# Optimization experiments

Measured on AMD Instinct MI355X. Metric: run time of the kernel, lower is better.

## Reference

```python
import jax, jax.numpy as jnp
import numpy as np

N_USERS = 50000
N0, N1, N2 = 200000, 50000, 12500
E0, E1, E2 = 1600000, 400000, 100000
B = 128
NUMP, TWEET, CATP, DES = 6, 768, 2, 768
IN_DIM, HID = 128, 128
SLOPE = 0.01  # LeakyReLU default


def setup_inputs() -> dict:
    key = jax.random.key(0)
    ks = iter(jax.random.split(key, 32))
    f32 = jnp.float32
    nrm = lambda s, sc=0.05: jax.random.normal(next(ks), s, f32) * sc
    inp = {}
    inp['x_raw'] = jax.random.normal(next(ks), (N_USERS, NUMP + TWEET + CATP + DES), f32)
    inp['W_des'] = nrm((DES, IN_DIM // 4)); inp['b_des'] = jnp.zeros((IN_DIM // 4,), f32)
    inp['W_tweet'] = nrm((TWEET, IN_DIM // 4)); inp['b_tweet'] = jnp.zeros((IN_DIM // 4,), f32)
    inp['W_num'] = nrm((NUMP, IN_DIM // 4)); inp['b_num'] = jnp.zeros((IN_DIM // 4,), f32)
    inp['W_cat'] = nrm((CATP, IN_DIM // 4)); inp['b_cat'] = jnp.zeros((IN_DIM // 4,), f32)
    inp['W_in'] = nrm((IN_DIM, HID)); inp['b_in'] = jnp.zeros((HID,), f32)
    inp['prelu_a'] = jnp.full((HID,), 0.25, f32)
    inp['W_conv'] = nrm((3, HID, HID)); inp['b_conv'] = jnp.zeros((3, HID), f32)
    inp['Wc1'] = nrm((3 * HID, HID)); inp['bc1'] = jnp.zeros((HID,), f32)
    inp['Wc2'] = nrm((HID, HID)); inp['bc2'] = jnp.zeros((HID,), f32)
    ri = lambda n, hi: jax.random.randint(next(ks), (n,), 0, hi, jnp.int32)
    inp['nodelist'] = ri(N0, N_USERS)
    inp['e0'] = jnp.stack([ri(E0, N0), ri(E0, N0)])
    inp['e1'] = jnp.stack([ri(E1, N1), ri(E1, N1)])
    inp['e2'] = jnp.stack([ri(E2, N2), ri(E2, N2)])
    inp['parent1'] = ri(N0, N1)   # coarsening assignment layer0 -> layer1
    inp['parent2'] = ri(N1, N2)   # layer1 -> layer2
    inp['batch1'] = jnp.sort(ri(N1, B))
    inp['batch2'] = jnp.sort(ri(N2, B))
    return inp


def _leaky(x):
    return jnp.where(x > 0, x, SLOPE * x)


def _gcn(h, ei, W, b, n):
    # GCNConv: lin -> sym-normalized add-aggregation with self-loops -> +bias
    h = h @ W
    loop = jnp.arange(n, dtype=ei.dtype)
    src = jnp.concatenate([ei[0], loop])
    dst = jnp.concatenate([ei[1], loop])
    deg = jax.ops.segment_sum(jnp.ones(dst.shape, h.dtype), dst, num_segments=n)
    dinv = jnp.where(deg > 0, jax.lax.rsqrt(deg), 0.0)
    msg = h[src] * (dinv[src] * dinv[dst])[:, None]
    return jax.ops.segment_sum(msg, dst, num_segments=n) + b


def reference(x_raw, W_des, b_des, W_tweet, b_tweet, W_num, b_num, W_cat, b_cat,
              W_in, b_in, prelu_a, W_conv, b_conv, Wc1, bc1, Wc2, bc2,
              nodelist, e0, e1, e2, parent1, parent2, batch1, batch2):
    # FeatureEncoder (twibot-20 slicing order: num_prop | tweet | cat_prop | des)
    n = _leaky(x_raw[:, :NUMP] @ W_num + b_num)
    t = _leaky(x_raw[:, NUMP:NUMP + TWEET] @ W_tweet + b_tweet)
    c = _leaky(x_raw[:, NUMP + TWEET:NUMP + TWEET + CATP] @ W_cat + b_cat)
    d = _leaky(x_raw[:, NUMP + TWEET + CATP:] @ W_des + b_des)
    h = jnp.concatenate([d, t, n, c], axis=1) @ W_in + b_in
    enc = jnp.where(h > 0, h, prelu_a * h)  # PReLU

    x = enc[nodelist]  # [N0, HID] gather per batched nodelists
    edges = [e0, e1, e2]
    sizes = [N0, N1, N2]
    parents = [parent1, parent2]
    nxt = [N1, N2]
    xs = []
    for i in range(3):
        x = jax.nn.relu(_gcn(x, edges[i], W_conv[i], b_conv[i], sizes[i]))
        if i < 2:  # SEPooling: pure scatter-add onto parent nodes (nn unused in its forward)
            x = jax.nn.relu(jax.ops.segment_sum(x, parents[i], num_segments=nxt[i]))
        xs.append(x)
    pooled = jnp.concatenate([
        jax.ops.segment_sum(xs[0], batch1, num_segments=B),
        jax.ops.segment_sum(xs[1], batch2, num_segments=B),
        jax.ops.segment_sum(xs[2], batch2, num_segments=B),
    ], axis=1)  # global sum pool, batch at layer min(i+1, tree_depth-1)
    z = jax.nn.relu(pooled @ Wc1 + bc1)  # dropout inactive (eval)
    return z @ Wc2 + bc2
```

## Files before the change

kernel.cpp:

```cpp
#include <hip/hip_runtime.h>

#define N_USERS 50000
#define NN0 200000
#define NN1 50000
#define NN2 12500
#define EE0 1600000
#define EE1 400000
#define EE2 100000


__global__ __launch_bounds__(256) void k_enc3(
    const float* __restrict__ xr,
    const float* __restrict__ Wd, const float* __restrict__ bd,
    const float* __restrict__ Wt, const float* __restrict__ bt,
    const float* __restrict__ Wn, const float* __restrict__ bn,
    const float* __restrict__ Wc, const float* __restrict__ bc,
    float* __restrict__ h128)
{
    __shared__ float XsB[4368];
    __shared__ float Ws[32][68];
    __shared__ float xnc[64][8];
    __shared__ float Wl[8][64];

    int t = threadIdx.x;
    int lane = t & 63, wv = t >> 6;
    int cg = t & 15, rg = t >> 4;
    int base = blockIdx.x * 64;

    if (t < 64) {
        int row = base + t;
        if (row < N_USERS) {
            const float* xp = xr + (size_t)row * 1544;
            float4 a = *(const float4*)xp;
            float2 b2 = *(const float2*)(xp + 4);
            float2 c2 = *(const float2*)(xp + 774);
            xnc[t][0] = a.x; xnc[t][1] = a.y; xnc[t][2] = a.z; xnc[t][3] = a.w;
            xnc[t][4] = b2.x; xnc[t][5] = b2.y; xnc[t][6] = c2.x; xnc[t][7] = c2.y;
        } else {
            #pragma unroll
            for (int k = 0; k < 8; k++) xnc[t][k] = 0.f;
        }
    } else if (t >= 192) {
        int l = t - 192;
        #pragma unroll
        for (int k = 0; k < 8; k++) {
            float w = 0.f;
            if (l < 32) { if (k < 6) w = Wn[k * 32 + l]; }
            else        { if (k >= 6) w = Wc[(k - 6) * 32 + (l - 32)]; }
            Wl[k][l] = w;
        }
    }

    int srow = (lane & 15) + wv * 16;
    int grow = base + srow;
    bool vrow = grow < N_USERS;
    const float* xrow = xr + (size_t)grow * 1544;

    float acc[4][4];
    #pragma unroll
    for (int r = 0; r < 4; r++)
        #pragma unroll
        for (int c = 0; c < 4; c++) acc[r][c] = 0.f;

    for (int kc = 0; kc < 768; kc += 32) {
        __syncthreads();
        #pragma unroll
        for (int h = 0; h < 2; h++) {
            int q = (lane >> 4) + h * 4;
            float4 vd = {0.f, 0.f, 0.f, 0.f};
            float2 va = {0.f, 0.f}, vb = {0.f, 0.f};
            if (vrow) {
                const float* xp = xrow + kc + q * 4;
                vd = *(const float4*)(xp + 776);
                va = *(const float2*)(xp + 6);
                vb = *(const float2*)(xp + 8);
            }
            int k0 = q * 4;
            XsB[(k0 + 0) * 68 + srow] = vd.x;
            XsB[(k0 + 1) * 68 + srow] = vd.y;
            XsB[(k0 + 2) * 68 + srow] = vd.z;
            XsB[(k0 + 3) * 68 + srow] = vd.w;
            XsB[2192 + (k0 + 0) * 68 + srow] = va.x;
            XsB[2192 + (k0 + 1) * 68 + srow] = va.y;
            XsB[2192 + (k0 + 2) * 68 + srow] = vb.x;
            XsB[2192 + (k0 + 3) * 68 + srow] = vb.y;
        }
        #pragma unroll
        for (int h = 0; h < 2; h++) {
            int fi = t + h * 256;
            int k = fi >> 4, c4 = (fi & 15) * 4;
            float4 w = (c4 < 32) ? *(const float4*)(Wd + (size_t)(kc + k) * 32 + c4)
                                 : *(const float4*)(Wt + (size_t)(kc + k) * 32 + (c4 - 32));
            *(float4*)&Ws[k][c4] = w;
        }
        __syncthreads();

        const float* Xp = (cg < 8) ? XsB : (XsB + 2192);
        #pragma unroll 8
        for (int k = 0; k < 32; k++) {
            float4 xv = *(const float4*)(Xp + k * 68 + rg * 4);
            float4 wv2 = *(const float4*)&Ws[k][cg * 4];
            acc[0][0] = fmaf(xv.x, wv2.x, acc[0][0]);
            acc[0][1] = fmaf(xv.x, wv2.y, acc[0][1]);
            acc[0][2] = fmaf(xv.x, wv2.z, acc[0][2]);
            acc[0][3] = fmaf(xv.x, wv2.w, acc[0][3]);
            acc[1][0] = fmaf(xv.y, wv2.x, acc[1][0]);
            acc[1][1] = fmaf(xv.y, wv2.y, acc[1][1]);
            acc[1][2] = fmaf(xv.y, wv2.z, acc[1][2]);
            acc[1][3] = fmaf(xv.y, wv2.w, acc[1][3]);
            acc[2][0] = fmaf(xv.z, wv2.x, acc[2][0]);
            acc[2][1] = fmaf(xv.z, wv2.y, acc[2][1]);
            acc[2][2] = fmaf(xv.z, wv2.z, acc[2][2]);
            acc[2][3] = fmaf(xv.z, wv2.w, acc[2][3]);
            acc[3][0] = fmaf(xv.w, wv2.x, acc[3][0]);
            acc[3][1] = fmaf(xv.w, wv2.y, acc[3][1]);
            acc[3][2] = fmaf(xv.w, wv2.z, acc[3][2]);
            acc[3][3] = fmaf(xv.w, wv2.w, acc[3][3]);
        }
    }

    float bh[4], bl[4], wlv[8][4];
    #pragma unroll
    for (int c = 0; c < 4; c++) {
        int j = cg * 4 + c;
        bh[c] = (j < 32) ? bd[j] : bt[j - 32];
        bl[c] = (j < 32) ? bn[j] : bc[j - 32];
        #pragma unroll
        for (int k = 0; k < 8; k++) wlv[k][c] = Wl[k][j];
    }
    #pragma unroll
    for (int r = 0; r < 4; r++) {
        int lr = rg * 4 + r;
        int row = base + lr;
        if (row >= N_USERS) break;
        float4 hv;
        float* ph = &hv.x;
        #pragma unroll
        for (int c = 0; c < 4; c++) {
            float v = acc[r][c] + bh[c];
            ph[c] = v > 0.f ? v : 0.01f * v;
        }
        *(float4*)(h128 + (size_t)row * 128 + cg * 4) = hv;
        float4 lv;
        float* pl = &lv.x;
        #pragma unroll
        for (int c = 0; c < 4; c++) {
            float v = bl[c];
            #pragma unroll
            for (int k = 0; k < 8; k++) v = fmaf(xnc[lr][k], wlv[k][c], v);
            pl[c] = v > 0.f ? v : 0.01f * v;
        }
        *(float4*)(h128 + (size_t)row * 128 + 64 + cg * 4) = lv;
    }
}

__global__ __launch_bounds__(256) void k_gemm2(
    const float* __restrict__ X, const float* __restrict__ W1,
    const float* __restrict__ b1, const float* __restrict__ pa,
    const float* __restrict__ W2, float* __restrict__ OUT, int n)
{
    __shared__ float Xs[32][132];
    __shared__ float Ws[32][132];
    int t = threadIdx.x;
    int cg = t & 31, rg = t >> 5;
    int base = blockIdx.x * 32;

    #pragma unroll
    for (int h = 0; h < 4; h++) {
        int fi = t + h * 256;
        int row = fi >> 5, q = fi & 31;
        float4 v = {0.f, 0.f, 0.f, 0.f};
        if (base + row < n) v = *(const float4*)(X + (size_t)(base + row) * 128 + q * 4);
        *(float4*)&Xs[row][q * 4] = v;
    }

    float acc[4][4];
    #pragma unroll
    for (int r = 0; r < 4; r++)
        #pragma unroll
        for (int c = 0; c < 4; c++) acc[r][c] = 0.f;

    for (int kc = 0; kc < 128; kc += 32) {
        __syncthreads();
        #pragma unroll
        for (int h = 0; h < 4; h++) {
            int fi = t + h * 256;
            int k = fi >> 5, q = fi & 31;
            *(float4*)&Ws[k][q * 4] = *(const float4*)(W1 + (size_t)(kc + k) * 128 + q * 4);
        }
        __syncthreads();
        #pragma unroll
        for (int k4 = 0; k4 < 8; k4++) {
            int k = k4 * 4;
            float4 w0 = *(const float4*)&Ws[k + 0][cg * 4];
            float4 w1 = *(const float4*)&Ws[k + 1][cg * 4];
            float4 w2 = *(const float4*)&Ws[k + 2][cg * 4];
            float4 w3 = *(const float4*)&Ws[k + 3][cg * 4];
            #pragma unroll
            for (int r = 0; r < 4; r++) {
                float4 xv = *(const float4*)&Xs[rg * 4 + r][kc + k];
                acc[r][0] = fmaf(xv.w, w3.x, fmaf(xv.z, w2.x, fmaf(xv.y, w1.x, fmaf(xv.x, w0.x, acc[r][0]))));
                acc[r][1] = fmaf(xv.w, w3.y, fmaf(xv.z, w2.y, fmaf(xv.y, w1.y, fmaf(xv.x, w0.y, acc[r][1]))));
                acc[r][2] = fmaf(xv.w, w3.z, fmaf(xv.z, w2.z, fmaf(xv.y, w1.z, fmaf(xv.x, w0.z, acc[r][2]))));
                acc[r][3] = fmaf(xv.w, w3.w, fmaf(xv.z, w2.w, fmaf(xv.y, w1.w, fmaf(xv.x, w0.w, acc[r][3]))));
            }
        }
    }

    float4 bv = *(const float4*)(b1 + cg * 4);
    float4 pv = *(const float4*)(pa + cg * 4);
    __syncthreads();
    #pragma unroll
    for (int r = 0; r < 4; r++) {
        float v0 = acc[r][0] + bv.x; v0 = v0 > 0.f ? v0 : pv.x * v0;
        float v1 = acc[r][1] + bv.y; v1 = v1 > 0.f ? v1 : pv.y * v1;
        float v2 = acc[r][2] + bv.z; v2 = v2 > 0.f ? v2 : pv.z * v2;
        float v3 = acc[r][3] + bv.w; v3 = v3 > 0.f ? v3 : pv.w * v3;
        Xs[rg * 4 + r][cg * 4 + 0] = v0;
        Xs[rg * 4 + r][cg * 4 + 1] = v1;
        Xs[rg * 4 + r][cg * 4 + 2] = v2;
        Xs[rg * 4 + r][cg * 4 + 3] = v3;
        acc[r][0] = 0.f; acc[r][1] = 0.f; acc[r][2] = 0.f; acc[r][3] = 0.f;
    }

    for (int kc = 0; kc < 128; kc += 32) {
        __syncthreads();
        #pragma unroll
        for (int h = 0; h < 4; h++) {
            int fi = t + h * 256;
            int k = fi >> 5, q = fi & 31;
            *(float4*)&Ws[k][q * 4] = *(const float4*)(W2 + (size_t)(kc + k) * 128 + q * 4);
        }
        __syncthreads();
        #pragma unroll
        for (int k4 = 0; k4 < 8; k4++) {
            int k = k4 * 4;
            float4 w0 = *(const float4*)&Ws[k + 0][cg * 4];
            float4 w1 = *(const float4*)&Ws[k + 1][cg * 4];
            float4 w2 = *(const float4*)&Ws[k + 2][cg * 4];
            float4 w3 = *(const float4*)&Ws[k + 3][cg * 4];
            #pragma unroll
            for (int r = 0; r < 4; r++) {
                float4 xv = *(const float4*)&Xs[rg * 4 + r][kc + k];
                acc[r][0] = fmaf(xv.w, w3.x, fmaf(xv.z, w2.x, fmaf(xv.y, w1.x, fmaf(xv.x, w0.x, acc[r][0]))));
                acc[r][1] = fmaf(xv.w, w3.y, fmaf(xv.z, w2.y, fmaf(xv.y, w1.y, fmaf(xv.x, w0.y, acc[r][1]))));
                acc[r][2] = fmaf(xv.w, w3.z, fmaf(xv.z, w2.z, fmaf(xv.y, w1.z, fmaf(xv.x, w0.z, acc[r][2]))));
                acc[r][3] = fmaf(xv.w, w3.w, fmaf(xv.z, w2.w, fmaf(xv.y, w1.w, fmaf(xv.x, w0.w, acc[r][3]))));
            }
        }
    }

    #pragma unroll
    for (int r = 0; r < 4; r++) {
        int row = base + rg * 4 + r;
        if (row >= n) break;
        float4 v;
        v.x = acc[r][0]; v.y = acc[r][1]; v.z = acc[r][2]; v.w = acc[r][3];
        *(float4*)(OUT + (size_t)row * 128 + cg * 4) = v;
    }
}

__global__ __launch_bounds__(256) void k_gemmT(
    const float* X, const float* __restrict__ W, float* OUT, int n)
{
    __shared__ float Xs[32][132];
    __shared__ float Ws[32][132];
    int t = threadIdx.x;
    int cg = t & 31, rg = t >> 5;
    int base = blockIdx.x * 32;

    #pragma unroll
    for (int h = 0; h < 4; h++) {
        int fi = t + h * 256;
        int row = fi >> 5, q = fi & 31;
        float4 v = {0.f, 0.f, 0.f, 0.f};
        if (base + row < n) v = *(const float4*)(X + (size_t)(base + row) * 128 + q * 4);
        *(float4*)&Xs[row][q * 4] = v;
    }

    float acc[4][4];
    #pragma unroll
    for (int r = 0; r < 4; r++)
        #pragma unroll
        for (int c = 0; c < 4; c++) acc[r][c] = 0.f;

    for (int kc = 0; kc < 128; kc += 32) {
        __syncthreads();
        #pragma unroll
        for (int h = 0; h < 4; h++) {
            int fi = t + h * 256;
            int k = fi >> 5, q = fi & 31;
            *(float4*)&Ws[k][q * 4] = *(const float4*)(W + (size_t)(kc + k) * 128 + q * 4);
        }
        __syncthreads();
        #pragma unroll
        for (int k4 = 0; k4 < 8; k4++) {
            int k = k4 * 4;
            float4 w0 = *(const float4*)&Ws[k + 0][cg * 4];
            float4 w1 = *(const float4*)&Ws[k + 1][cg * 4];
            float4 w2 = *(const float4*)&Ws[k + 2][cg * 4];
            float4 w3 = *(const float4*)&Ws[k + 3][cg * 4];
            #pragma unroll
            for (int r = 0; r < 4; r++) {
                float4 xv = *(const float4*)&Xs[rg * 4 + r][kc + k];
                acc[r][0] = fmaf(xv.w, w3.x, fmaf(xv.z, w2.x, fmaf(xv.y, w1.x, fmaf(xv.x, w0.x, acc[r][0]))));
                acc[r][1] = fmaf(xv.w, w3.y, fmaf(xv.z, w2.y, fmaf(xv.y, w1.y, fmaf(xv.x, w0.y, acc[r][1]))));
                acc[r][2] = fmaf(xv.w, w3.z, fmaf(xv.z, w2.z, fmaf(xv.y, w1.z, fmaf(xv.x, w0.z, acc[r][2]))));
                acc[r][3] = fmaf(xv.w, w3.w, fmaf(xv.z, w2.w, fmaf(xv.y, w1.w, fmaf(xv.x, w0.w, acc[r][3]))));
            }
        }
    }

    #pragma unroll
    for (int r = 0; r < 4; r++) {
        int row = base + rg * 4 + r;
        if (row >= n) break;
        float4 v;
        v.x = acc[r][0]; v.y = acc[r][1]; v.z = acc[r][2]; v.w = acc[r][3];
        *(float4*)(OUT + (size_t)row * 128 + cg * 4) = v;
    }
}

__device__ __forceinline__ void seg_of_scanblk(int b, int& doff, int& bsoff, int& lb) {
    if (b < 196)      { doff = 0;      bsoff = 0;   lb = b; }
    else if (b < 245) { doff = 200704; bsoff = 196; lb = b - 196; }
    else if (b < 258) { doff = 250880; bsoff = 245; lb = b - 245; }
    else if (b < 307) { doff = 264192; bsoff = 258; lb = b - 258; }
    else              { doff = 314368; bsoff = 307; lb = b - 307; }
}

__global__ __launch_bounds__(256) void k_count_all(
    const int* __restrict__ d0, const int* __restrict__ d1, const int* __restrict__ d2,
    const int* __restrict__ p1, const int* __restrict__ p2,
    int* __restrict__ degs, int* __restrict__ ranks)
{
    int t0 = blockIdx.x * 256 + threadIdx.x;
    if (t0 >= 587500) return;
    #pragma unroll
    for (int k = 0; k < 4; k++) {
        int gid = t0 + k * 587500;
        int idx;
        if (gid < 1600000)      idx = d0[gid];
        else if (gid < 2000000) idx = 200704 + d1[gid - 1600000];
        else if (gid < 2100000) idx = 250880 + d2[gid - 2000000];
        else if (gid < 2300000) idx = 264192 + p1[gid - 2100000];
        else                    idx = 314368 + p2[gid - 2300000];
        ranks[gid] = atomicAdd(&degs[idx], 1);
    }
}

__global__ __launch_bounds__(256) void k_scan_all(
    const int* __restrict__ degs, int* __restrict__ rowsts, int* __restrict__ bsums)
{
    __shared__ int sh[256];
    int doff, bsoff, lb;
    seg_of_scanblk(blockIdx.x, doff, bsoff, lb);
    int t = threadIdx.x;
    int base = doff + lb * 1024 + t * 4;
    int v[4], s = 0;
    #pragma unroll
    for (int k = 0; k < 4; k++) { v[k] = degs[base + k]; s += v[k]; }
    sh[t] = s;
    __syncthreads();
    for (int off = 1; off < 256; off <<= 1) {
        int x = 0;
        if (t >= off) x = sh[t - off];
        __syncthreads();
        if (t >= off) sh[t] += x;
        __syncthreads();
    }
    int ex = sh[t] - s;
    if (t == 255) bsums[bsoff + lb] = sh[255];
    #pragma unroll
    for (int k = 0; k < 4; k++) { rowsts[base + k] = ex; ex += v[k]; }
}

__global__ __launch_bounds__(256) void k_scanadd_all(
    int* __restrict__ rowsts, const int* __restrict__ bsums,
    const int* __restrict__ degs, float* __restrict__ dinvs)
{
    __shared__ int sh[256];
    int doff, bsoff, lb;
    seg_of_scanblk(blockIdx.x, doff, bsoff, lb);
    int t = threadIdx.x;
    sh[t] = (t < lb) ? bsums[bsoff + t] : 0;
    __syncthreads();
    #pragma unroll
    for (int off = 128; off >= 1; off >>= 1) {
        if (t < off) sh[t] += sh[t + off];
        __syncthreads();
    }
    int add = sh[0];
    int base = doff + lb * 1024 + t * 4;
    bool dodinv = (doff <= 250880);
    #pragma unroll
    for (int k = 0; k < 4; k++) {
        int i = base + k;
        rowsts[i] += add;
        if (dodinv) dinvs[i] = rsqrtf((float)degs[i] + 1.0f);
    }
}

__global__ __launch_bounds__(256) void k_scatter_all(
    const int* __restrict__ s0, const int* __restrict__ d0,
    const int* __restrict__ s1, const int* __restrict__ d1,
    const int* __restrict__ s2, const int* __restrict__ d2,
    const int* __restrict__ p1, const int* __restrict__ p2,
    const int* __restrict__ nl, const float* __restrict__ dinvs,
    const int* __restrict__ rowsts, const int* __restrict__ ranks,
    int* __restrict__ elists, float* __restrict__ edw)
{
    int t0 = blockIdx.x * 256 + threadIdx.x;
    if (t0 >= 587500) return;
    #pragma unroll
    for (int k = 0; k < 4; k++) {
        int gid = t0 + k * 587500;
        if (gid < 1600000) {
            int s = s0[gid];
            int p = rowsts[d0[gid]] + ranks[gid];
            elists[p] = nl[s];
            edw[p] = dinvs[s];
        } else if (gid < 2000000) {
            int i = gid - 1600000;
            int s = s1[i];
            int p = rowsts[200704 + d1[i]] + ranks[gid];
            elists[1600000 + p] = s;
            edw[1600000 + p] = dinvs[200704 + s];
        } else if (gid < 2100000) {
            int i = gid - 2000000;
            int s = s2[i];
            int p = rowsts[250880 + d2[i]] + ranks[gid];
            elists[2000000 + p] = s;
            edw[2000000 + p] = dinvs[250880 + s];
        } else if (gid < 2300000) {
            int i = gid - 2100000;
            int p = rowsts[264192 + p1[i]] + ranks[gid];
            elists[2100000 + p] = i;
        } else {
            int i = gid - 2300000;
            int p = rowsts[314368 + p2[i]] + ranks[gid];
            elists[2300000 + p] = i;
        }
    }
}

__global__ __launch_bounds__(256) void k_gatherU(
    const float* __restrict__ U, const int* __restrict__ nl,
    const int* __restrict__ rowst, const int* __restrict__ elist,
    const float* __restrict__ edw, const float* __restrict__ dinv,
    const float* __restrict__ bias, float* __restrict__ out, int n)
{
    size_t gid = (size_t)blockIdx.x * 256 + threadIdx.x;
    int d = (int)(gid >> 5);
    if (d >= n) return;
    int l = (int)(gid & 31);
    const float4* Uv = (const float4*)U;
    float dd = dinv[d];
    float4 self = Uv[(size_t)nl[d] * 32 + l];
    float4 acc;
    acc.x = self.x * dd; acc.y = self.y * dd; acc.z = self.z * dd; acc.w = self.w * dd;
    int s0 = rowst[d], s1 = rowst[d + 1];
    for (int e = s0; e < s1; ++e) {
        int srow = elist[e];
        float w = edw[e];
        float4 v = Uv[(size_t)srow * 32 + l];
        acc.x = fmaf(v.x, w, acc.x);
        acc.y = fmaf(v.y, w, acc.y);
        acc.z = fmaf(v.z, w, acc.z);
        acc.w = fmaf(v.w, w, acc.w);
    }
    const float4 b = ((const float4*)bias)[l];
    float4 y;
    y.x = fmaxf(fmaf(acc.x, dd, b.x), 0.f);
    y.y = fmaxf(fmaf(acc.y, dd, b.y), 0.f);
    y.z = fmaxf(fmaf(acc.z, dd, b.z), 0.f);
    y.w = fmaxf(fmaf(acc.w, dd, b.w), 0.f);
    ((float4*)out)[(size_t)d * 32 + l] = y;
}

__global__ __launch_bounds__(256) void k_gather(
    const float* __restrict__ h, const int* __restrict__ rowst,
    const int* __restrict__ elist, const float* __restrict__ edw,
    const float* __restrict__ dinv, const float* __restrict__ bias,
    float* __restrict__ out, int n)
{
    size_t gid = (size_t)blockIdx.x * 256 + threadIdx.x;
    int d = (int)(gid >> 5);
    if (d >= n) return;
    int l = (int)(gid & 31);
    const float4* hv = (const float4*)h;
    float dd = dinv[d];
    float4 self = hv[(size_t)d * 32 + l];
    float4 acc;
    acc.x = self.x * dd; acc.y = self.y * dd; acc.z = self.z * dd; acc.w = self.w * dd;
    int s0 = rowst[d], s1 = rowst[d + 1];
    for (int e = s0; e < s1; ++e) {
        int srow = elist[e];
        float w = edw[e];
        float4 v = hv[(size_t)srow * 32 + l];
        acc.x = fmaf(v.x, w, acc.x);
        acc.y = fmaf(v.y, w, acc.y);
        acc.z = fmaf(v.z, w, acc.z);
        acc.w = fmaf(v.w, w, acc.w);
    }
    const float4 b = ((const float4*)bias)[l];
    float4 y;
    y.x = fmaxf(fmaf(acc.x, dd, b.x), 0.f);
    y.y = fmaxf(fmaf(acc.y, dd, b.y), 0.f);
    y.z = fmaxf(fmaf(acc.z, dd, b.z), 0.f);
    y.w = fmaxf(fmaf(acc.w, dd, b.w), 0.f);
    ((float4*)out)[(size_t)d * 32 + l] = y;
}

__global__ __launch_bounds__(256) void k_poolgather(
    const float* __restrict__ Y, const int* __restrict__ rowst,
    const int* __restrict__ elist, float* __restrict__ out, int np)
{
    size_t gid = (size_t)blockIdx.x * 256 + threadIdx.x;
    int p = (int)(gid >> 5);
    if (p >= np) return;
    int l = (int)(gid & 31);
    const float4* yv = (const float4*)Y;
    float4 acc = {0.f, 0.f, 0.f, 0.f};
    int s0 = rowst[p], s1 = rowst[p + 1];
    for (int e = s0; e < s1; ++e) {
        int i = elist[e];
        float4 v = yv[(size_t)i * 32 + l];
        acc.x += v.x; acc.y += v.y; acc.z += v.z; acc.w += v.w;
    }
    float4 y;
    y.x = fmaxf(acc.x, 0.f); y.y = fmaxf(acc.y, 0.f);
    y.z = fmaxf(acc.z, 0.f); y.w = fmaxf(acc.w, 0.f);
    ((float4*)out)[(size_t)p * 32 + l] = y;
}

__global__ __launch_bounds__(128) void k_bpool_all(
    const float* __restrict__ X1, const float* __restrict__ X2, const float* __restrict__ Y2,
    const int* __restrict__ b1, const int* __restrict__ b2, float* __restrict__ pl)
{
    int b = blockIdx.x;
    const float* src; const int* bidx; int coloff, n, r0;
    if (b < 391)      { src = X1; bidx = b1; coloff = 0;   n = 50000; r0 = b * 128; }
    else if (b < 489) { src = X2; bidx = b2; coloff = 128; n = 12500; r0 = (b - 391) * 128; }
    else              { src = Y2; bidx = b2; coloff = 256; n = 12500; r0 = (b - 489) * 128; }
    if (r0 >= n) return;
    int j = threadIdx.x;
    int r1 = min(r0 + 128, n);
    float acc = 0.f;
    int prev = bidx[r0];
    for (int r = r0; r < r1; ++r) {
        int bb = bidx[r];
        if (bb != prev) {
            unsafeAtomicAdd(&pl[(size_t)prev * 384 + coloff + j], acc);
            acc = 0.f; prev = bb;
        }
        acc += src[(size_t)r * 128 + j];
    }
    unsafeAtomicAdd(&pl[(size_t)prev * 384 + coloff + j], acc);
}

__global__ void k_mlp2(const float* __restrict__ PL,
                       const float* __restrict__ Wc1, const float* __restrict__ bc1,
                       const float* __restrict__ Wc2, const float* __restrict__ bc2,
                       float* __restrict__ out)
{
    __shared__ float as[384];
    __shared__ float zs[128];
    int r = blockIdx.x, j = threadIdx.x;
    as[j] = PL[(size_t)r * 384 + j];
    as[j + 128] = PL[(size_t)r * 384 + 128 + j];
    as[j + 256] = PL[(size_t)r * 384 + 256 + j];
    __syncthreads();
    float acc = bc1[j];
    for (int k = 0; k < 384; k++) acc = fmaf(as[k], Wc1[(size_t)k * 128 + j], acc);
    zs[j] = fmaxf(acc, 0.f);
    __syncthreads();
    float o = bc2[j];
    for (int k = 0; k < 128; k++) o = fmaf(zs[k], Wc2[(size_t)k * 128 + j], o);
    out[(size_t)r * 128 + j] = o;
}

extern "C" void kernel_launch(void* const* d_in, const int* in_sizes, int n_in,
                              void* d_out, int out_size, void* d_ws, size_t ws_size,
                              hipStream_t stream)
{
    const float* x_raw  = (const float*)d_in[0];
    const float* W_des  = (const float*)d_in[1];
    const float* b_des  = (const float*)d_in[2];
    const float* W_twe  = (const float*)d_in[3];
    const float* b_twe  = (const float*)d_in[4];
    const float* W_num  = (const float*)d_in[5];
    const float* b_num  = (const float*)d_in[6];
    const float* W_cat  = (const float*)d_in[7];
    const float* b_cat  = (const float*)d_in[8];
    const float* W_in   = (const float*)d_in[9];
    const float* b_in   = (const float*)d_in[10];
    const float* prelua = (const float*)d_in[11];
    const float* W_conv = (const float*)d_in[12];
    const float* b_conv = (const float*)d_in[13];
    const float* Wc1    = (const float*)d_in[14];
    const float* bc1    = (const float*)d_in[15];
    const float* Wc2    = (const float*)d_in[16];
    const float* bc2    = (const float*)d_in[17];
    const int* nodelist = (const int*)d_in[18];
    const int* e0       = (const int*)d_in[19];
    const int* e1       = (const int*)d_in[20];
    const int* e2       = (const int*)d_in[21];
    const int* parent1  = (const int*)d_in[22];
    const int* parent2  = (const int*)d_in[23];
    const int* batch1   = (const int*)d_in[24];
    const int* batch2   = (const int*)d_in[25];

    float* WS  = (float*)d_ws;
    float* ENC = WS;
    int*   DEGS   = (int*)d_ws;
    int*   ROWSTS = DEGS + 327680;
    float* DINVS  = (float*)(ROWSTS + 327680);
    int*   BSUMS  = (int*)(DINVS + 264192);
    int*   RANKS  = BSUMS + 512;
    int*   ELISTS = RANKS + 2350000;
    float* U  = WS + 6400000;
    float* H  = WS + 12800000;
    float* Y  = WS + 19200000;
    float* X1 = WS + 44800000;
    float* X2 = WS + 51200000;
    float* PL = WS + 52800000;
    float* EDW = WS + 52900000;

    hipMemsetAsync(PL, 0, (size_t)128 * 384 * 4, stream);

    k_enc3<<<(N_USERS + 63) / 64, 256, 0, stream>>>(
        x_raw, W_des, b_des, W_twe, b_twe, W_num, b_num, W_cat, b_cat, ENC);
    k_gemm2<<<(N_USERS + 31) / 32, 256, 0, stream>>>(
        ENC, W_in, b_in, prelua, W_conv, U, N_USERS);

    hipMemsetAsync(DEGS, 0, (size_t)327680 * 4, stream);
    k_count_all<<<(587500 + 255) / 256, 256, 0, stream>>>(
        e0 + EE0, e1 + EE1, e2 + EE2, parent1, parent2, DEGS, RANKS);
    k_scan_all<<<320, 256, 0, stream>>>(DEGS, ROWSTS, BSUMS);
    k_scanadd_all<<<320, 256, 0, stream>>>(ROWSTS, BSUMS, DEGS, DINVS);
    k_scatter_all<<<(587500 + 255) / 256, 256, 0, stream>>>(
        e0, e0 + EE0, e1, e1 + EE1, e2, e2 + EE2, parent1, parent2,
        nodelist, DINVS, ROWSTS, RANKS, ELISTS, EDW);

    k_gatherU<<<(int)(((size_t)NN0 * 32 + 255) / 256), 256, 0, stream>>>(
        U, nodelist, ROWSTS, ELISTS, EDW, DINVS, b_conv, Y, NN0);
    k_poolgather<<<(int)(((size_t)NN1 * 32 + 255) / 256), 256, 0, stream>>>(
        Y, ROWSTS + 264192, ELISTS + 2100000, X1, NN1);

    k_gemmT<<<(NN1 + 31) / 32, 256, 0, stream>>>(X1, W_conv + 16384, H, NN1);
    k_gather<<<(int)(((size_t)NN1 * 32 + 255) / 256), 256, 0, stream>>>(
        H, ROWSTS + 200704, ELISTS + 1600000, EDW + 1600000, DINVS + 200704,
        b_conv + 128, Y, NN1);
    k_poolgather<<<(int)(((size_t)NN2 * 32 + 255) / 256), 256, 0, stream>>>(
        Y, ROWSTS + 314368, ELISTS + 2300000, X2, NN2);

    k_gemmT<<<(NN2 + 31) / 32, 256, 0, stream>>>(X2, W_conv + 32768, H, NN2);
    k_gather<<<(int)(((size_t)NN2 * 32 + 255) / 256), 256, 0, stream>>>(
        H, ROWSTS + 250880, ELISTS + 2000000, EDW + 2000000, DINVS + 250880,
        b_conv + 256, Y, NN2);

    k_bpool_all<<<587, 128, 0, stream>>>(X1, X2, Y, batch1, batch2, PL);

    k_mlp2<<<128, 128, 0, stream>>>(PL, Wc1, bc1, Wc2, bc2, (float*)d_out);
}
```

Baseline: 718.1 us.

## Co-schedule CSR build with encoder/GEMM kernels and emit GCN outputs in pooled-parent order

The degree-count atomics now run as extra blocks inside the encoder kernel, and the CSR scatter runs as extra blocks inside the two-layer GEMM kernel. This overlaps the independent graph preprocessing with dense compute and removes two launches. The GCN gather kernels now iterate through the parent-sorted child permutation and write rows in pooled order. The pooling step then sums contiguous rows instead of doing indirect gathers. The workspace layout is moved so the integer buffers no longer alias the encoder output, since the count kernel now runs at the same time as the encoder.

```diff
diff --git a/kernel.cpp b/kernel.cpp
--- a/kernel.cpp
+++ b/kernel.cpp
@@ -8,19 +8,43 @@
 #define EE1 400000
 #define EE2 100000
 
-
-__global__ __launch_bounds__(256) void k_enc3(
+#define ENC_BLOCKS 782
+#define CNT_BLOCKS 2295
+#define GM2_BLOCKS 1563
+
+
+__global__ __launch_bounds__(256) void k_enc_count(
     const float* __restrict__ xr,
     const float* __restrict__ Wd, const float* __restrict__ bd,
     const float* __restrict__ Wt, const float* __restrict__ bt,
     const float* __restrict__ Wn, const float* __restrict__ bn,
     const float* __restrict__ Wc, const float* __restrict__ bc,
-    float* __restrict__ h128)
+    float* __restrict__ h128,
+    const int* __restrict__ d0, const int* __restrict__ d1, const int* __restrict__ d2,
+    const int* __restrict__ p1, const int* __restrict__ p2,
+    int* __restrict__ degs, int* __restrict__ ranks)
 {
     __shared__ float XsB[4368];
     __shared__ float Ws[32][68];
     __shared__ float xnc[64][8];
     __shared__ float Wl[8][64];
+
+    if (blockIdx.x >= ENC_BLOCKS) {
+        int t0 = (blockIdx.x - ENC_BLOCKS) * 256 + threadIdx.x;
+        if (t0 >= 587500) return;
+        #pragma unroll
+        for (int k = 0; k < 4; k++) {
+            int gid = t0 + k * 587500;
+            int idx;
+            if (gid < 1600000)      idx = d0[gid];
+            else if (gid < 2000000) idx = 200704 + d1[gid - 1600000];
+            else if (gid < 2100000) idx = 250880 + d2[gid - 2000000];
+            else if (gid < 2300000) idx = 264192 + p1[gid - 2100000];
+            else                    idx = 314368 + p2[gid - 2300000];
+            ranks[gid] = atomicAdd(&degs[idx], 1);
+        }
+        return;
+    }
 
     int t = threadIdx.x;
     int lane = t & 63, wv = t >> 6;
@@ -154,13 +178,57 @@
     }
 }
 
-__global__ __launch_bounds__(256) void k_gemm2(
+__global__ __launch_bounds__(256) void k_gemm2_scatter(
     const float* __restrict__ X, const float* __restrict__ W1,
     const float* __restrict__ b1, const float* __restrict__ pa,
-    const float* __restrict__ W2, float* __restrict__ OUT, int n)
+    const float* __restrict__ W2, float* __restrict__ OUT, int n,
+    const int* __restrict__ s0, const int* __restrict__ d0,
+    const int* __restrict__ s1, const int* __restrict__ d1,
+    const int* __restrict__ s2, const int* __restrict__ d2,
+    const int* __restrict__ p1, const int* __restrict__ p2,
+    const int* __restrict__ nl, const float* __restrict__ dinvs,
+    const int* __restrict__ rowsts, const int* __restrict__ ranks,
+    int* __restrict__ elists, float* __restrict__ edw)
 {
     __shared__ float Xs[32][132];
-    __shared__ float Ws[32][132];
+    __shared__ float Wsh[32][132];
+
+    if (blockIdx.x >= GM2_BLOCKS) {
+        int t0 = (blockIdx.x - GM2_BLOCKS) * 256 + threadIdx.x;
+        if (t0 >= 587500) return;
+        #pragma unroll
+        for (int k = 0; k < 4; k++) {
+            int gid = t0 + k * 587500;
+            if (gid < 1600000) {
+                int s = s0[gid];
+                int p = rowsts[d0[gid]] + ranks[gid];
+                elists[p] = nl[s];
+                edw[p] = dinvs[s];
+            } else if (gid < 2000000) {
+                int i = gid - 1600000;
+                int s = s1[i];
+                int p = rowsts[200704 + d1[i]] + ranks[gid];
+                elists[1600000 + p] = s;
+                edw[1600000 + p] = dinvs[200704 + s];
+            } else if (gid < 2100000) {
+                int i = gid - 2000000;
+                int s = s2[i];
+                int p = rowsts[250880 + d2[i]] + ranks[gid];
+                elists[2000000 + p] = s;
+                edw[2000000 + p] = dinvs[250880 + s];
+            } else if (gid < 2300000) {
+                int i = gid - 2100000;
+                int p = rowsts[264192 + p1[i]] + ranks[gid];
+                elists[2100000 + p] = i;
+            } else {
+                int i = gid - 2300000;
+                int p = rowsts[314368 + p2[i]] + ranks[gid];
+                elists[2300000 + p] = i;
+            }
+        }
+        return;
+    }
+
     int t = threadIdx.x;
     int cg = t & 31, rg = t >> 5;
     int base = blockIdx.x * 32;
@@ -186,7 +254,111 @@
         for (int h = 0; h < 4; h++) {
             int fi = t + h * 256;
             int k = fi >> 5, q = fi & 31;
-            *(float4*)&Ws[k][q * 4] = *(const float4*)(W1 + (size_t)(kc + k) * 128 + q * 4);
+            *(float4*)&Wsh[k][q * 4] = *(const float4*)(W1 + (size_t)(kc + k) * 128 + q * 4);
+        }
+        __syncthreads();
+        #pragma unroll
+        for (int k4 = 0; k4 < 8; k4++) {
+            int k = k4 * 4;
+            float4 w0 = *(const float4*)&Wsh[k + 0][cg * 4];
+            float4 w1 = *(const float4*)&Wsh[k + 1][cg * 4];
+            float4 w2 = *(const float4*)&Wsh[k + 2][cg * 4];
+            float4 w3 = *(const float4*)&Wsh[k + 3][cg * 4];
+            #pragma unroll
+            for (int r = 0; r < 4; r++) {
+                float4 xv = *(const float4*)&Xs[rg * 4 + r][kc + k];
+                acc[r][0] = fmaf(xv.w, w3.x, fmaf(xv.z, w2.x, fmaf(xv.y, w1.x, fmaf(xv.x, w0.x, acc[r][0]))));
+                acc[r][1] = fmaf(xv.w, w3.y, fmaf(xv.z, w2.y, fmaf(xv.y, w1.y, fmaf(xv.x, w0.y, acc[r][1]))));
+                acc[r][2] = fmaf(xv.w, w3.z, fmaf(xv.z, w2.z, fmaf(xv.y, w1.z, fmaf(xv.x, w0.z, acc[r][2]))));
+                acc[r][3] = fmaf(xv.w, w3.w, fmaf(xv.z, w2.w, fmaf(xv.y, w1.w, fmaf(xv.x, w0.w, acc[r][3]))));
+            }
+        }
+    }
+
+    float4 bv = *(const float4*)(b1 + cg * 4);
+    float4 pv = *(const float4*)(pa + cg * 4);
+    __syncthreads();
+    #pragma unroll
+    for (int r = 0; r < 4; r++) {
+        float v0 = acc[r][0] + bv.x; v0 = v0 > 0.f ? v0 : pv.x * v0;
+        float v1 = acc[r][1] + bv.y; v1 = v1 > 0.f ? v1 : pv.y * v1;
+        float v2 = acc[r][2] + bv.z; v2 = v2 > 0.f ? v2 : pv.z * v2;
+        float v3 = acc[r][3] + bv.w; v3 = v3 > 0.f ? v3 : pv.w * v3;
+        Xs[rg * 4 + r][cg * 4 + 0] = v0;
+        Xs[rg * 4 + r][cg * 4 + 1] = v1;
+        Xs[rg * 4 + r][cg * 4 + 2] = v2;
+        Xs[rg * 4 + r][cg * 4 + 3] = v3;
+        acc[r][0] = 0.f; acc[r][1] = 0.f; acc[r][2] = 0.f; acc[r][3] = 0.f;
+    }
+
+    for (int kc = 0; kc < 128; kc += 32) {
+        __syncthreads();
+        #pragma unroll
+        for (int h = 0; h < 4; h++) {
+            int fi = t + h * 256;
+            int k = fi >> 5, q = fi & 31;
+            *(float4*)&Wsh[k][q * 4] = *(const float4*)(W2 + (size_t)(kc + k) * 128 + q * 4);
+        }
+        __syncthreads();
+        #pragma unroll
+        for (int k4 = 0; k4 < 8; k4++) {
+            int k = k4 * 4;
+            float4 w0 = *(const float4*)&Wsh[k + 0][cg * 4];
+            float4 w1 = *(const float4*)&Wsh[k + 1][cg * 4];
+            float4 w2 = *(const float4*)&Wsh[k + 2][cg * 4];
+            float4 w3 = *(const float4*)&Wsh[k + 3][cg * 4];
+            #pragma unroll
+            for (int r = 0; r < 4; r++) {
+                float4 xv = *(const float4*)&Xs[rg * 4 + r][kc + k];
+                acc[r][0] = fmaf(xv.w, w3.x, fmaf(xv.z, w2.x, fmaf(xv.y, w1.x, fmaf(xv.x, w0.x, acc[r][0]))));
+                acc[r][1] = fmaf(xv.w, w3.y, fmaf(xv.z, w2.y, fmaf(xv.y, w1.y, fmaf(xv.x, w0.y, acc[r][1]))));
+                acc[r][2] = fmaf(xv.w, w3.z, fmaf(xv.z, w2.z, fmaf(xv.y, w1.z, fmaf(xv.x, w0.z, acc[r][2]))));
+                acc[r][3] = fmaf(xv.w, w3.w, fmaf(xv.z, w2.w, fmaf(xv.y, w1.w, fmaf(xv.x, w0.w, acc[r][3]))));
+            }
+        }
+    }
+
+    #pragma unroll
+    for (int r = 0; r < 4; r++) {
+        int row = base + rg * 4 + r;
+        if (row >= n) break;
+        float4 v;
+        v.x = acc[r][0]; v.y = acc[r][1]; v.z = acc[r][2]; v.w = acc[r][3];
+        *(float4*)(OUT + (size_t)row * 128 + cg * 4) = v;
+    }
+}
+
+__global__ __launch_bounds__(256) void k_gemmT(
+    const float* X, const float* __restrict__ W, float* OUT, int n)
+{
+    __shared__ float Xs[32][132];
+    __shared__ float Ws[32][132];
+    int t = threadIdx.x;
+    int cg = t & 31, rg = t >> 5;
+    int base = blockIdx.x * 32;
+
+    #pragma unroll
+    for (int h = 0; h < 4; h++) {
+        int fi = t + h * 256;
+        int row = fi >> 5, q = fi & 31;
+        float4 v = {0.f, 0.f, 0.f, 0.f};
+        if (base + row < n) v = *(const float4*)(X + (size_t)(base + row) * 128 + q * 4);
+        *(float4*)&Xs[row][q * 4] = v;
+    }
+
+    float acc[4][4];
+    #pragma unroll
+    for (int r = 0; r < 4; r++)
+        #pragma unroll
+        for (int c = 0; c < 4; c++) acc[r][c] = 0.f;
+
+    for (int kc = 0; kc < 128; kc += 32) {
+        __syncthreads();
+        #pragma unroll
+        for (int h = 0; h < 4; h++) {
+            int fi = t + h * 256;
+            int k = fi >> 5, q = fi & 31;
+            *(float4*)&Ws[k][q * 4] = *(const float4*)(W + (size_t)(kc + k) * 128 + q * 4);
         }
         __syncthreads();
         #pragma unroll
@@ -207,49 +379,6 @@
         }
     }
 
-    float4 bv = *(const float4*)(b1 + cg * 4);
-    float4 pv = *(const float4*)(pa + cg * 4);
-    __syncthreads();
-    #pragma unroll
-    for (int r = 0; r < 4; r++) {
-        float v0 = acc[r][0] + bv.x; v0 = v0 > 0.f ? v0 : pv.x * v0;
-        float v1 = acc[r][1] + bv.y; v1 = v1 > 0.f ? v1 : pv.y * v1;
-        float v2 = acc[r][2] + bv.z; v2 = v2 > 0.f ? v2 : pv.z * v2;
-        float v3 = acc[r][3] + bv.w; v3 = v3 > 0.f ? v3 : pv.w * v3;
-        Xs[rg * 4 + r][cg * 4 + 0] = v0;
-        Xs[rg * 4 + r][cg * 4 + 1] = v1;
-        Xs[rg * 4 + r][cg * 4 + 2] = v2;
-        Xs[rg * 4 + r][cg * 4 + 3] = v3;
-        acc[r][0] = 0.f; acc[r][1] = 0.f; acc[r][2] = 0.f; acc[r][3] = 0.f;
-    }
-
-    for (int kc = 0; kc < 128; kc += 32) {
-        __syncthreads();
-        #pragma unroll
-        for (int h = 0; h < 4; h++) {
-            int fi = t + h * 256;
-            int k = fi >> 5, q = fi & 31;
-            *(float4*)&Ws[k][q * 4] = *(const float4*)(W2 + (size_t)(kc + k) * 128 + q * 4);
-        }
-        __syncthreads();
-        #pragma unroll
-        for (int k4 = 0; k4 < 8; k4++) {
-            int k = k4 * 4;
-            float4 w0 = *(const float4*)&Ws[k + 0][cg * 4];
-            float4 w1 = *(const float4*)&Ws[k + 1][cg * 4];
-            float4 w2 = *(const float4*)&Ws[k + 2][cg * 4];
-            float4 w3 = *(const float4*)&Ws[k + 3][cg * 4];
-            #pragma unroll
-            for (int r = 0; r < 4; r++) {
-                float4 xv = *(const float4*)&Xs[rg * 4 + r][kc + k];
-                acc[r][0] = fmaf(xv.w, w3.x, fmaf(xv.z, w2.x, fmaf(xv.y, w1.x, fmaf(xv.x, w0.x, acc[r][0]))));
-                acc[r][1] = fmaf(xv.w, w3.y, fmaf(xv.z, w2.y, fmaf(xv.y, w1.y, fmaf(xv.x, w0.y, acc[r][1]))));
-                acc[r][2] = fmaf(xv.w, w3.z, fmaf(xv.z, w2.z, fmaf(xv.y, w1.z, fmaf(xv.x, w0.z, acc[r][2]))));
-                acc[r][3] = fmaf(xv.w, w3.w, fmaf(xv.z, w2.w, fmaf(xv.y, w1.w, fmaf(xv.x, w0.w, acc[r][3]))));
-            }
-        }
-    }
-
     #pragma unroll
     for (int r = 0; r < 4; r++) {
         int row = base + rg * 4 + r;
@@ -260,67 +389,6 @@
     }
 }
 
-__global__ __launch_bounds__(256) void k_gemmT(
-    const float* X, const float* __restrict__ W, float* OUT, int n)
-{
-    __shared__ float Xs[32][132];
-    __shared__ float Ws[32][132];
-    int t = threadIdx.x;
-    int cg = t & 31, rg = t >> 5;
-    int base = blockIdx.x * 32;
-
-    #pragma unroll
-    for (int h = 0; h < 4; h++) {
-        int fi = t + h * 256;
-        int row = fi >> 5, q = fi & 31;
-        float4 v = {0.f, 0.f, 0.f, 0.f};
-        if (base + row < n) v = *(const float4*)(X + (size_t)(base + row) * 128 + q * 4);
-        *(float4*)&Xs[row][q * 4] = v;
-    }
-
-    float acc[4][4];
-    #pragma unroll
-    for (int r = 0; r < 4; r++)
-        #pragma unroll
-        for (int c = 0; c < 4; c++) acc[r][c] = 0.f;
-
-    for (int kc = 0; kc < 128; kc += 32) {
-        __syncthreads();
-        #pragma unroll
-        for (int h = 0; h < 4; h++) {
-            int fi = t + h * 256;
-            int k = fi >> 5, q = fi & 31;
-            *(float4*)&Ws[k][q * 4] = *(const float4*)(W + (size_t)(kc + k) * 128 + q * 4);
-        }
-        __syncthreads();
-        #pragma unroll
-        for (int k4 = 0; k4 < 8; k4++) {
-            int k = k4 * 4;
-            float4 w0 = *(const float4*)&Ws[k + 0][cg * 4];
-            float4 w1 = *(const float4*)&Ws[k + 1][cg * 4];
-            float4 w2 = *(const float4*)&Ws[k + 2][cg * 4];
-            float4 w3 = *(const float4*)&Ws[k + 3][cg * 4];
-            #pragma unroll
-            for (int r = 0; r < 4; r++) {
-                float4 xv = *(const float4*)&Xs[rg * 4 + r][kc + k];
-                acc[r][0] = fmaf(xv.w, w3.x, fmaf(xv.z, w2.x, fmaf(xv.y, w1.x, fmaf(xv.x, w0.x, acc[r][0]))));
-                acc[r][1] = fmaf(xv.w, w3.y, fmaf(xv.z, w2.y, fmaf(xv.y, w1.y, fmaf(xv.x, w0.y, acc[r][1]))));
-                acc[r][2] = fmaf(xv.w, w3.z, fmaf(xv.z, w2.z, fmaf(xv.y, w1.z, fmaf(xv.x, w0.z, acc[r][2]))));
-                acc[r][3] = fmaf(xv.w, w3.w, fmaf(xv.z, w2.w, fmaf(xv.y, w1.w, fmaf(xv.x, w0.w, acc[r][3]))));
-            }
-        }
-    }
-
-    #pragma unroll
-    for (int r = 0; r < 4; r++) {
-        int row = base + rg * 4 + r;
-        if (row >= n) break;
-        float4 v;
-        v.x = acc[r][0]; v.y = acc[r][1]; v.z = acc[r][2]; v.w = acc[r][3];
-        *(float4*)(OUT + (size_t)row * 128 + cg * 4) = v;
-    }
-}
-
 __device__ __forceinline__ void seg_of_scanblk(int b, int& doff, int& bsoff, int& lb) {
     if (b < 196)      { doff = 0;      bsoff = 0;   lb = b; }
     else if (b < 245) { doff = 200704; bsoff = 196; lb = b - 196; }
@@ -329,26 +397,6 @@
     else              { doff = 314368; bsoff = 307; lb = b - 307; }
 }
 
-__global__ __launch_bounds__(256) void k_count_all(
-    const int* __restrict__ d0, const int* __restrict__ d1, const int* __restrict__ d2,
-    const int* __restrict__ p1, const int* __restrict__ p2,
-    int* __restrict__ degs, int* __restrict__ ranks)
-{
-    int t0 = blockIdx.x * 256 + threadIdx.x;
-    if (t0 >= 587500) return;
-    #pragma unroll
-    for (int k = 0; k < 4; k++) {
-        int gid = t0 + k * 587500;
-        int idx;
-        if (gid < 1600000)      idx = d0[gid];
-        else if (gid < 2000000) idx = 200704 + d1[gid - 1600000];
-        else if (gid < 2100000) idx = 250880 + d2[gid - 2000000];
-        else if (gid < 2300000) idx = 264192 + p1[gid - 2100000];
-        else                    idx = 314368 + p2[gid - 2300000];
-        ranks[gid] = atomicAdd(&degs[idx], 1);
-    }
-}
-
 __global__ __launch_bounds__(256) void k_scan_all(
     const int* __restrict__ degs, int* __restrict__ rowsts, int* __restrict__ bsums)
 {
@@ -401,59 +449,18 @@
     }
 }
 
-__global__ __launch_bounds__(256) void k_scatter_all(
-    const int* __restrict__ s0, const int* __restrict__ d0,
-    const int* __restrict__ s1, const int* __restrict__ d1,
-    const int* __restrict__ s2, const int* __restrict__ d2,
-    const int* __restrict__ p1, const int* __restrict__ p2,
-    const int* __restrict__ nl, const float* __restrict__ dinvs,
-    const int* __restrict__ rowsts, const int* __restrict__ ranks,
-    int* __restrict__ elists, float* __restrict__ edw)
-{
-    int t0 = blockIdx.x * 256 + threadIdx.x;
-    if (t0 >= 587500) return;
-    #pragma unroll
-    for (int k = 0; k < 4; k++) {
-        int gid = t0 + k * 587500;
-        if (gid < 1600000) {
-            int s = s0[gid];
-            int p = rowsts[d0[gid]] + ranks[gid];
-            elists[p] = nl[s];
-            edw[p] = dinvs[s];
-        } else if (gid < 2000000) {
-            int i = gid - 1600000;
-            int s = s1[i];
-            int p = rowsts[200704 + d1[i]] + ranks[gid];
-            elists[1600000 + p] = s;
-            edw[1600000 + p] = dinvs[200704 + s];
-        } else if (gid < 2100000) {
-            int i = gid - 2000000;
-            int s = s2[i];
-            int p = rowsts[250880 + d2[i]] + ranks[gid];
-            elists[2000000 + p] = s;
-            edw[2000000 + p] = dinvs[250880 + s];
-        } else if (gid < 2300000) {
-            int i = gid - 2100000;
-            int p = rowsts[264192 + p1[i]] + ranks[gid];
-            elists[2100000 + p] = i;
-        } else {
-            int i = gid - 2300000;
-            int p = rowsts[314368 + p2[i]] + ranks[gid];
-            elists[2300000 + p] = i;
-        }
-    }
-}
-
-__global__ __launch_bounds__(256) void k_gatherU(
+__global__ __launch_bounds__(256) void k_gatherU_perm(
     const float* __restrict__ U, const int* __restrict__ nl,
     const int* __restrict__ rowst, const int* __restrict__ elist,
     const float* __restrict__ edw, const float* __restrict__ dinv,
-    const float* __restrict__ bias, float* __restrict__ out, int n)
+    const float* __restrict__ bias, const int* __restrict__ perm,
+    float* __restrict__ out, int n)
 {
     size_t gid = (size_t)blockIdx.x * 256 + threadIdx.x;
-    int d = (int)(gid >> 5);
-    if (d >= n) return;
+    int i = (int)(gid >> 5);
+    if (i >= n) return;
     int l = (int)(gid & 31);
+    int d = perm[i];
     const float4* Uv = (const float4*)U;
     float dd = dinv[d];
     float4 self = Uv[(size_t)nl[d] * 32 + l];
@@ -475,19 +482,20 @@
     y.y = fmaxf(fmaf(acc.y, dd, b.y), 0.f);
     y.z = fmaxf(fmaf(acc.z, dd, b.z), 0.f);
     y.w = fmaxf(fmaf(acc.w, dd, b.w), 0.f);
-    ((float4*)out)[(size_t)d * 32 + l] = y;
-}
-
-__global__ __launch_bounds__(256) void k_gather(
+    ((float4*)out)[(size_t)i * 32 + l] = y;
+}
+
+__global__ __launch_bounds__(256) void k_gather_perm(
     const float* __restrict__ h, const int* __restrict__ rowst,
     const int* __restrict__ elist, const float* __restrict__ edw,
     const float* __restrict__ dinv, const float* __restrict__ bias,
-    float* __restrict__ out, int n)
+    const int* __restrict__ perm, float* __restrict__ out, int n)
 {
     size_t gid = (size_t)blockIdx.x * 256 + threadIdx.x;
-    int d = (int)(gid >> 5);
-    if (d >= n) return;
+    int i = (int)(gid >> 5);
+    if (i >= n) return;
     int l = (int)(gid & 31);
+    int d = perm ? perm[i] : i;
     const float4* hv = (const float4*)h;
     float dd = dinv[d];
     float4 self = hv[(size_t)d * 32 + l];
@@ -509,23 +517,22 @@
     y.y = fmaxf(fmaf(acc.y, dd, b.y), 0.f);
     y.z = fmaxf(fmaf(acc.z, dd, b.z), 0.f);
     y.w = fmaxf(fmaf(acc.w, dd, b.w), 0.f);
-    ((float4*)out)[(size_t)d * 32 + l] = y;
-}
-
-__global__ __launch_bounds__(256) void k_poolgather(
-    const float* __restrict__ Y, const int* __restrict__ rowst,
-    const int* __restrict__ elist, float* __restrict__ out, int np)
+    ((float4*)out)[(size_t)i * 32 + l] = y;
+}
+
+__global__ __launch_bounds__(256) void k_poolseq(
+    const float* __restrict__ Yp, const int* __restrict__ prowst,
+    float* __restrict__ out, int np)
 {
     size_t gid = (size_t)blockIdx.x * 256 + threadIdx.x;
     int p = (int)(gid >> 5);
     if (p >= np) return;
     int l = (int)(gid & 31);
-    const float4* yv = (const float4*)Y;
+    const float4* yv = (const float4*)Yp;
     float4 acc = {0.f, 0.f, 0.f, 0.f};
-    int s0 = rowst[p], s1 = rowst[p + 1];
-    for (int e = s0; e < s1; ++e) {
-        int i = elist[e];
-        float4 v = yv[(size_t)i * 32 + l];
+    int c0 = prowst[p], c1 = prowst[p + 1];
+    for (int c = c0; c < c1; ++c) {
+        float4 v = yv[(size_t)c * 32 + l];
         acc.x += v.x; acc.y += v.y; acc.z += v.z; acc.w += v.w;
     }
     float4 y;
@@ -613,52 +620,52 @@
 
     float* WS  = (float*)d_ws;
     float* ENC = WS;
-    int*   DEGS   = (int*)d_ws;
+    float* U   = WS + 6400000;
+    float* H   = WS + 12800000;
+    float* Y   = WS + 19200000;
+    float* X1  = WS + 44800000;
+    float* X2  = WS + 51200000;
+    float* PL  = WS + 52800000;
+    float* EDW = WS + 52900000;
+    int*   DEGS   = (int*)(WS + 55000000);
     int*   ROWSTS = DEGS + 327680;
     float* DINVS  = (float*)(ROWSTS + 327680);
     int*   BSUMS  = (int*)(DINVS + 264192);
     int*   RANKS  = BSUMS + 512;
     int*   ELISTS = RANKS + 2350000;
-    float* U  = WS + 6400000;
-    float* H  = WS + 12800000;
-    float* Y  = WS + 19200000;
-    float* X1 = WS + 44800000;
-    float* X2 = WS + 51200000;
-    float* PL = WS + 52800000;
-    float* EDW = WS + 52900000;
 
     hipMemsetAsync(PL, 0, (size_t)128 * 384 * 4, stream);
-
-    k_enc3<<<(N_USERS + 63) / 64, 256, 0, stream>>>(
-        x_raw, W_des, b_des, W_twe, b_twe, W_num, b_num, W_cat, b_cat, ENC);
-    k_gemm2<<<(N_USERS + 31) / 32, 256, 0, stream>>>(
-        ENC, W_in, b_in, prelua, W_conv, U, N_USERS);
-
     hipMemsetAsync(DEGS, 0, (size_t)327680 * 4, stream);
-    k_count_all<<<(587500 + 255) / 256, 256, 0, stream>>>(
+
+    k_enc_count<<<ENC_BLOCKS + CNT_BLOCKS, 256, 0, stream>>>(
+        x_raw, W_des, b_des, W_twe, b_twe, W_num, b_num, W_cat, b_cat, ENC,
         e0 + EE0, e1 + EE1, e2 + EE2, parent1, parent2, DEGS, RANKS);
+
     k_scan_all<<<320, 256, 0, stream>>>(DEGS, ROWSTS, BSUMS);
     k_scanadd_all<<<320, 256, 0, stream>>>(ROWSTS, BSUMS, DEGS, DINVS);
-    k_scatter_all<<<(587500 + 255) / 256, 256, 0, stream>>>(
+
+    k_gemm2_scatter<<<GM2_BLOCKS + CNT_BLOCKS, 256, 0, stream>>>(
+        ENC, W_in, b_in, prelua, W_conv, U, N_USERS,
         e0, e0 + EE0, e1, e1 + EE1, e2, e2 + EE2, parent1, parent2,
         nodelist, DINVS, ROWSTS, RANKS, ELISTS, EDW);
 
-    k_gatherU<<<(int)(((size_t)NN0 * 32 + 255) / 256), 256, 0, stream>>>(
-        U, nodelist, ROWSTS, ELISTS, EDW, DINVS, b_conv, Y, NN0);
-    k_poolgather<<<(int)(((size_t)NN1 * 32 + 255) / 256), 256, 0, stream>>>(
-        Y, ROWSTS + 264192, ELISTS + 2100000, X1, NN1);
+    k_gatherU_perm<<<(int)(((size_t)NN0 * 32 + 255) / 256), 256, 0, stream>>>(
+        U, nodelist, ROWSTS, ELISTS, EDW, DINVS, b_conv,
+        ELISTS + 2100000, Y, NN0);
+    k_poolseq<<<(int)(((size_t)NN1 * 32 + 255) / 256), 256, 0, stream>>>(
+        Y, ROWSTS + 264192, X1, NN1);
 
     k_gemmT<<<(NN1 + 31) / 32, 256, 0, stream>>>(X1, W_conv + 16384, H, NN1);
-    k_gather<<<(int)(((size_t)NN1 * 32 + 255) / 256), 256, 0, stream>>>(
+    k_gather_perm<<<(int)(((size_t)NN1 * 32 + 255) / 256), 256, 0, stream>>>(
         H, ROWSTS + 200704, ELISTS + 1600000, EDW + 1600000, DINVS + 200704,
-        b_conv + 128, Y, NN1);
-    k_poolgather<<<(int)(((size_t)NN2 * 32 + 255) / 256), 256, 0, stream>>>(
-        Y, ROWSTS + 314368, ELISTS + 2300000, X2, NN2);
+        b_conv + 128, ELISTS + 2300000, Y, NN1);
+    k_poolseq<<<(int)(((size_t)NN2 * 32 + 255) / 256), 256, 0, stream>>>(
+        Y, ROWSTS + 314368, X2, NN2);
 
     k_gemmT<<<(NN2 + 31) / 32, 256, 0, stream>>>(X2, W_conv + 32768, H, NN2);
-    k_gather<<<(int)(((size_t)NN2 * 32 + 255) / 256), 256, 0, stream>>>(
+    k_gather_perm<<<(int)(((size_t)NN2 * 32 + 255) / 256), 256, 0, stream>>>(
         H, ROWSTS + 250880, ELISTS + 2000000, EDW + 2000000, DINVS + 250880,
-        b_conv + 256, Y, NN2);
+        b_conv + 256, nullptr, Y, NN2);
 
     k_bpool_all<<<587, 128, 0, stream>>>(X1, X2, Y, batch1, batch2, PL);
 
```

New measurement: 646.9 us, median of 2. 1.11x faster.
